# Kernel optimization log

Hardware: AMD Instinct MI355X
Metric: run time of the kernel (lower is better)

## Reference

```python
import jax, jax.numpy as jnp
import numpy as np
import math

# dims (match init_kwargs / input_specs)
T, B, S = 2048, 8, 512
D, H, DFF, NQ, W = 512, 8, 2048, 10, 16
EPS = 1e-5
NEG = -1e30


def _ln(x, g, b):
    mu = jnp.mean(x, axis=-1, keepdims=True)
    var = jnp.mean((x - mu) ** 2, axis=-1, keepdims=True)
    return (x - mu) * jax.lax.rsqrt(var + EPS) * g + b


def setup_inputs() -> dict:
    key = jax.random.key(0)
    ks = jax.random.split(key, 10)
    f = lambda k, shape, s=0.02: jax.random.normal(k, shape, jnp.float32) * s
    return {
        'tgt': jax.random.normal(ks[0], (T, B, D), jnp.float32),
        'memory': jax.random.normal(ks[1], (S, B, D), jnp.float32),
        'queries': f(ks[2], (NQ, D), 1.0 / math.sqrt(D)),
        'wk': f(ks[3], (NQ, 1), 1.0 / math.sqrt(NQ)),
        'in_proj_w': f(ks[4], (3 * D, D)),
        'in_proj_b': jnp.zeros((3 * D,), jnp.float32),
        'out_proj_w': f(ks[5], (D, D)),
        'out_proj_b': jnp.zeros((D,), jnp.float32),
        'lin1_w': f(ks[6], (DFF, D)),
        'lin1_b': jnp.zeros((DFF,), jnp.float32),
        'lin2_w': f(ks[7], (D, DFF)),
        'lin2_b': jnp.zeros((D,), jnp.float32),
        'ln1_g': jnp.ones((D,), jnp.float32), 'ln1_b': jnp.zeros((D,), jnp.float32),
        'ln2_g': jnp.ones((D,), jnp.float32), 'ln2_b': jnp.zeros((D,), jnp.float32),
        'ln3_g': jnp.ones((D,), jnp.float32), 'ln3_b': jnp.zeros((D,), jnp.float32),
    }


def _qa_block(x, queries, wk):
    # x: (T, B, D). Learned queries: per-head unit-norm + depth scale (QaN).
    dh = D // H
    q = queries.reshape(NQ, H, dh)
    q = q / (jnp.linalg.norm(q, axis=-1, keepdims=True) + 1e-6)
    q = (q / math.sqrt(dh)).reshape(NQ, D)
    # LocalAttention(window=W, look_backward=1, look_forward=1, non-causal, autopad)
    # k = v = x; T % W == 0 so autopad is a no-op.
    xb = jnp.transpose(x, (1, 0, 2))                       # (B, T, D)
    nw = T // W
    scale = D ** -0.5                                      # dim_head = D (single-head local attn)
    bk = xb.reshape(B, nw, W, D)
    pad = jnp.zeros((B, 1, W, D), x.dtype)
    bkp = jnp.concatenate([pad, bk, pad], axis=1)          # (B, nw+2, W, D)
    kv = jnp.concatenate([bkp[:, i:i + nw] for i in range(3)], axis=2)  # (B, nw, 3W, D)
    win_ok = jnp.pad(jnp.ones((nw,), bool), (1, 1))
    vm = jnp.stack([win_ok[i:i + nw] for i in range(3)], axis=1)        # (nw, 3)
    kmask = jnp.repeat(vm, W, axis=1)                                   # (nw, 3W)
    # The query vector is identical for every time step, so every position in a
    # window sees the same (query, keyset) pair -> one attention row per (n, window).
    sim = jnp.einsum('nd,bmjd->bnmj', q * scale, kv)       # (B, NQ, nw, 3W)
    sim = jnp.where(kmask[None, None], sim, NEG)
    attn = jax.nn.softmax(sim, axis=-1)
    out = jnp.einsum('bnmj,bmjd->bnmd', attn, kv)          # (B, NQ, nw, D)
    out = jnp.einsum('bnmd,n->bmd', out, wk[:, 0])         # mix N queries via wk (N,1)
    out = jnp.broadcast_to(out[:, :, None], (B, nw, W, D)).reshape(B, T, D)
    return jnp.transpose(out, (1, 0, 2))                   # (T, B, D)


def _mha_block(x, mem, in_w, in_b, out_w, out_b):
    dh = D // H
    wq, wkk, wv = jnp.split(in_w, 3, axis=0)
    bq, bk, bv = jnp.split(in_b, 3)
    q = (x @ wq.T + bq).reshape(T, B, H, dh).transpose(1, 2, 0, 3)   # (B,H,T,dh)
    k = (mem @ wkk.T + bk).reshape(S, B, H, dh).transpose(1, 2, 0, 3)
    v = (mem @ wv.T + bv).reshape(S, B, H, dh).transpose(1, 2, 0, 3)
    attn = jax.nn.softmax(jnp.einsum('bhtd,bhsd->bhts', q, k) / math.sqrt(dh), axis=-1)
    o = jnp.einsum('bhts,bhsd->bhtd', attn, v).transpose(2, 0, 1, 3).reshape(T, B, D)
    return o @ out_w.T + out_b


def reference(tgt, memory, queries, wk, in_proj_w, in_proj_b, out_proj_w, out_proj_b,
              lin1_w, lin1_b, lin2_w, lin2_b, ln1_g, ln1_b, ln2_g, ln2_b, ln3_g, ln3_b):
    # post-norm (norm_first=False), eval mode: dropouts + stochastic_depth(rate=0) are identity
    x = tgt
    x = _ln(x + _qa_block(x, queries, wk), ln1_g, ln1_b)
    x = _ln(x + _mha_block(x, memory, in_proj_w, in_proj_b, out_proj_w, out_proj_b), ln2_g, ln2_b)
    ff = jax.nn.relu(x @ lin1_w.T + lin1_b) @ lin2_w.T + lin2_b
    x = _ln(x + ff, ln3_g, ln3_b)
    # x = tgt + stochastic_depth(x - tgt) == x in eval / rate 0
    return x
```

## Files before the change

kernel.cpp:

```cpp
#include <hip/hip_runtime.h>


typedef unsigned short u16;
typedef unsigned int u32;
typedef short short8_t __attribute__((ext_vector_type(8)));
typedef float f32x4 __attribute__((ext_vector_type(4)));

#define TT 2048
#define BB 8
#define SS 512
#define DD 512
#define HH 8
#define DH 64
#define DFF 2048
#define NQ 10
#define WW 16
#define NW 128
#define KVPART 2097152

__device__ __forceinline__ float b2f(u16 u) {
    return __uint_as_float(((unsigned int)u) << 16);
}
__device__ __forceinline__ u16 f2b(float f) {
    unsigned int x = __float_as_uint(f);
    unsigned int r = x + 0x7FFFu + ((x >> 16) & 1u);
    return (u16)(r >> 16);
}
__device__ __forceinline__ u32 cvt_pk_bf16(float lo, float hi) {
    u32 r;
    asm volatile("v_cvt_pk_bf16_f32 %0, %1, %2" : "=v"(r) : "v"(lo), "v"(hi));
    return r;
}
__device__ __forceinline__ float wave_sum(float v) {
    #pragma unroll
    for (int o = 32; o > 0; o >>= 1) v += __shfl_xor(v, o, 64);
    return v;
}
__device__ __forceinline__ float wave_max(float v) {
    #pragma unroll
    for (int o = 32; o > 0; o >>= 1) v = fmaxf(v, __shfl_xor(v, o, 64));
    return v;
}
__device__ __forceinline__ void load4(const u16* p, float* v) {
    ushort4 t = *(const ushort4*)p;
    v[0] = b2f(t.x); v[1] = b2f(t.y); v[2] = b2f(t.z); v[3] = b2f(t.w);
}
__device__ __forceinline__ void load4(const float* p, float* v) {
    float4 t = *(const float4*)p;
    v[0] = t.x; v[1] = t.y; v[2] = t.z; v[3] = t.w;
}
__device__ __forceinline__ void st1(u16* p, float v) { *p = f2b(v); }
__device__ __forceinline__ void st1(float* p, float v) { *p = v; }

__device__ __forceinline__ void async16(const u16* g, u16* l) {
    __builtin_amdgcn_global_load_lds((const __attribute__((address_space(1))) u32*)g,
                                     (__attribute__((address_space(3))) u32*)l, 16, 0, 0);
}

__device__ __forceinline__ void xcd_remap(int& bx, int& by) {
    int flat = blockIdx.y * gridDim.x + blockIdx.x;
    int xcd = flat & 7;
    int j = flat >> 3;
    by = xcd * ((int)gridDim.y >> 3) + j / (int)gridDim.x;
    bx = j % (int)gridDim.x;
}

__device__ __forceinline__ void cvt_block(const float* s, u16* d, int base) {
    int i = base + threadIdx.x * 4;
    float4 v = *(const float4*)(s + i);
    ushort4 o;
    o.x = f2b(v.x); o.y = f2b(v.y); o.z = f2b(v.z); o.w = f2b(v.w);
    *(ushort4*)(d + i) = o;
}

__global__ __launch_bounds__(256) void cvt2_kernel(const float* __restrict__ s0,
                                                   const float* __restrict__ s1,
                                                   u16* __restrict__ d0,
                                                   u16* __restrict__ d1) {
    int bid = blockIdx.x;
    if (bid < 2048) cvt_block(s0, d0, bid * 1024);
    else            cvt_block(s1, d1, (bid - 2048) * 1024);
}

__global__ __launch_bounds__(256) void cvt3_kernel(const float* __restrict__ s0,
                                                   const float* __restrict__ s1,
                                                   const float* __restrict__ s2,
                                                   u16* __restrict__ d0,
                                                   u16* __restrict__ d1,
                                                   u16* __restrict__ d2) {
    int bid = blockIdx.x;
    if (bid < 256)       cvt_block(s0, d0, bid * 1024);
    else if (bid < 1280) cvt_block(s1, d1, (bid - 256) * 1024);
    else                 cvt_block(s2, d2, (bid - 1280) * 1024);
}

__global__ __launch_bounds__(512) void qeff_kernel(const float* __restrict__ queries,
                                                   float* __restrict__ qeff) {
    int d = threadIdx.x;
    const float KS = 0.0055242717280199026f;
    for (int n = 0; n < NQ; n++) {
        float v = queries[n * DD + d];
        float ss = wave_sum(v * v);
        float norm = sqrtf(ss);
        qeff[n * DD + d] = v / (norm + 1e-6f) * KS;
    }
}

__global__ __launch_bounds__(256) void p_kernel(const float* __restrict__ x,
                                                const float* __restrict__ qeff,
                                                float* __restrict__ p) {
    __shared__ float qe[NQ * DD];
    for (int i = threadIdx.x; i < NQ * DD; i += 256) qe[i] = qeff[i];
    __syncthreads();
    int b = blockIdx.x >> 9;
    int t = ((blockIdx.x & 511) << 2) + (threadIdx.x >> 6);
    int lane = threadIdx.x & 63;
    const float* xr = x + ((size_t)t * BB + b) * DD;
    float acc[NQ];
    #pragma unroll
    for (int n = 0; n < NQ; n++) acc[n] = 0.f;
    #pragma unroll
    for (int c = 0; c < 8; c++) {
        int d = c * 64 + lane;
        float xv = xr[d];
        #pragma unroll
        for (int n = 0; n < NQ; n++) acc[n] += xv * qe[n * DD + d];
    }
    #pragma unroll
    for (int n = 0; n < NQ; n++) {
        float s = wave_sum(acc[n]);
        if (lane == 0) p[((size_t)(b * NQ + n)) * TT + t] = s;
    }
}

__global__ __launch_bounds__(256) void winmix_kernel(const float* __restrict__ p,
                                                     const float* __restrict__ wk,
                                                     const float* __restrict__ x,
                                                     float* __restrict__ mixed) {
    __shared__ float As[48];
    int id = blockIdx.x;
    int b = id >> 7, m = id & 127;
    if (threadIdx.x < 64) {
        int j = threadIdx.x;
        int tj = (m - 1) * WW + j;
        bool valid = (j < 48) && (tj >= 0) && (tj < TT);
        float acc = 0.f;
        for (int n = 0; n < NQ; n++) {
            float v = valid ? p[((size_t)(b * NQ + n)) * TT + tj] : -1e30f;
            float mx = wave_max(v);
            float e = valid ? __expf(v - mx) : 0.f;
            float s = wave_sum(e);
            acc += wk[n] * (e / s);
        }
        if (j < 48) As[j] = acc;
    }
    __syncthreads();
    int d0 = threadIdx.x, d1 = threadIdx.x + 256;
    float a0 = 0.f, a1 = 0.f;
    int tb = (m - 1) * WW;
    for (int j = 0; j < 48; j++) {
        int t = tb + j;
        if ((unsigned)t < (unsigned)TT) {
            float aj = As[j];
            const float* xr = x + ((size_t)t * BB + b) * DD;
            a0 += aj * xr[d0];
            a1 += aj * xr[d1];
        }
    }
    mixed[(size_t)id * DD + d0] = a0;
    mixed[(size_t)id * DD + d1] = a1;
}

__global__ __launch_bounds__(256) void ln_qa_kernel(const float* __restrict__ a,
                                                    const float* __restrict__ mixed,
                                                    const float* __restrict__ g,
                                                    const float* __restrict__ bt,
                                                    u16* __restrict__ out) {
    int r = blockIdx.x * 4 + (threadIdx.x >> 6);
    int lane = threadIdx.x & 63;
    int t = r >> 3, b = r & 7;
    const float* ar = a + (size_t)r * DD;
    const float* mr = mixed + ((size_t)(b * NW + (t >> 4))) * DD;
    int d0 = lane * 8;
    float av[8], mv[8], gg[8], bb[8];
    load4(ar + d0, av); load4(ar + d0 + 4, av + 4);
    load4(mr + d0, mv); load4(mr + d0 + 4, mv + 4);
    load4(g + d0, gg);  load4(g + d0 + 4, gg + 4);
    load4(bt + d0, bb); load4(bt + d0 + 4, bb + 4);
    float v[8];
    float s = 0.f, s2 = 0.f;
    #pragma unroll
    for (int u = 0; u < 8; u++) { v[u] = av[u] + mv[u]; s += v[u]; s2 += v[u] * v[u]; }
    s = wave_sum(s); s2 = wave_sum(s2);
    float mu = s * (1.f / DD);
    float var = s2 * (1.f / DD) - mu * mu;
    float rs = rsqrtf(var + 1e-5f);
    #pragma unroll
    for (int u = 0; u < 8; u++) out[(size_t)r * DD + d0 + u] = f2b((v[u] - mu) * rs * gg[u] + bb[u]);
}

template <typename OT>
__global__ __launch_bounds__(256) void ln_rows_kernel(const u16* __restrict__ a,
                                                      const u16* __restrict__ bsrc,
                                                      const float* __restrict__ g,
                                                      const float* __restrict__ bt,
                                                      OT* __restrict__ out) {
    int r = blockIdx.x * 4 + (threadIdx.x >> 6);
    int lane = threadIdx.x & 63;
    const u16* ar = a + (size_t)r * DD;
    const u16* br = bsrc + (size_t)r * DD;
    int d0 = lane * 8;
    float av[8], cv[8], gg[8], bb[8];
    load4(ar + d0, av); load4(ar + d0 + 4, av + 4);
    load4(br + d0, cv); load4(br + d0 + 4, cv + 4);
    load4(g + d0, gg);  load4(g + d0 + 4, gg + 4);
    load4(bt + d0, bb); load4(bt + d0 + 4, bb + 4);
    float v[8];
    float s = 0.f, s2 = 0.f;
    #pragma unroll
    for (int u = 0; u < 8; u++) { v[u] = av[u] + cv[u]; s += v[u]; s2 += v[u] * v[u]; }
    s = wave_sum(s); s2 = wave_sum(s2);
    float mu = s * (1.f / DD);
    float var = s2 * (1.f / DD) - mu * mu;
    float rs = rsqrtf(var + 1e-5f);
    #pragma unroll
    for (int u = 0; u < 8; u++) st1(out + (size_t)r * DD + d0 + u, (v[u] - mu) * rs * gg[u] + bb[u]);
}

template <int RELU, int MT, int KV>
__global__ __launch_bounds__(256) void gemm_lds(const u16* __restrict__ A,
                                                const u16* __restrict__ W,
                                                const float* __restrict__ bias,
                                                u16* __restrict__ C,
                                                int M, int N, int K) {
    constexpr int BM = MT * 32;
    constexpr int NIA = BM / 64;
    __shared__ u16 As[2][BM * 32];
    __shared__ u16 Bs[2][128 * 32];
    int tid = threadIdx.x;
    int w = tid >> 6, lane = tid & 63;
    int n16 = lane & 15, quad = lane >> 4;
    int m0 = blockIdx.y * BM, n0 = blockIdx.x * 128;
    int wm16 = (w >> 1) * MT;
    int wn = (w & 1) * 64;

    const u16* gA[NIA];
    u16* lA[NIA];
    #pragma unroll
    for (int i = 0; i < NIA; i++) {
        int s = (w * NIA + i) * 64 + lane;
        int mb = s >> 6, kseg = (s >> 4) & 3, m = s & 15;
        gA[i] = A + (size_t)(m0 + mb * 16 + m) * K + kseg * 8;
        lA[i] = &As[0][(size_t)((w * NIA + i) * 64) * 8];
    }
    const u16* gB[2];
    u16* lB[2];
    #pragma unroll
    for (int i = 0; i < 2; i++) {
        int s = (w * 2 + i) * 64 + lane;
        int nb = s >> 6, kseg = (s >> 4) & 3, n = s & 15;
        gB[i] = W + (size_t)(n0 + nb * 16 + n) * K + kseg * 8;
        lB[i] = &Bs[0][(size_t)((w * 2 + i) * 64) * 8];
    }

    f32x4 acc[MT][4];
    #pragma unroll
    for (int i = 0; i < MT; i++)
        #pragma unroll
        for (int j = 0; j < 4; j++) acc[i][j] = (f32x4){0.f, 0.f, 0.f, 0.f};

    const int nk = K >> 5;
    #pragma unroll
    for (int i = 0; i < NIA; i++) async16(gA[i], lA[i]);
    #pragma unroll
    for (int i = 0; i < 2; i++) async16(gB[i], lB[i]);
    __syncthreads();

    for (int t = 0; t < nk; t++) {
        int cur = t & 1;
        if (t + 1 < nk) {
            int nxt = cur ^ 1;
            #pragma unroll
            for (int i = 0; i < NIA; i++) async16(gA[i] + (t + 1) * 32, lA[i] + nxt * (BM * 32));
            #pragma unroll
            for (int i = 0; i < 2; i++) async16(gB[i] + (t + 1) * 32, lB[i] + nxt * 4096);
        }
        const u16* Ac = &As[cur][0];
        const u16* Bc = &Bs[cur][0];
        short8_t af[MT], bf[4];
        #pragma unroll
        for (int im = 0; im < MT; im++)
            af[im] = *(const short8_t*)(Ac + (size_t)((wm16 + im) * 64 + lane) * 8);
        #pragma unroll
        for (int in = 0; in < 4; in++)
            bf[in] = *(const short8_t*)(Bc + (size_t)(((w & 1) * 4 + in) * 64 + lane) * 8);
        #pragma unroll
        for (int im = 0; im < MT; im++)
            #pragma unroll
            for (int in = 0; in < 4; in++)
                acc[im][in] = __builtin_amdgcn_mfma_f32_16x16x32_bf16(af[im], bf[in], acc[im][in], 0, 0, 0);
        __syncthreads();
    }

    float bia[4];
    #pragma unroll
    for (int in = 0; in < 4; in++) bia[in] = bias[n0 + wn + in * 16 + n16];
    #pragma unroll
    for (int im = 0; im < MT; im++) {
        #pragma unroll
        for (int r = 0; r < 4; r++) {
            int row = m0 + (wm16 + im) * 16 + quad * 4 + r;
            #pragma unroll
            for (int in = 0; in < 4; in++) {
                float v = acc[im][in][r] + bia[in];
                if (RELU) v = fmaxf(v, 0.f);
                if (KV) {
                    int col = n0 + wn + in * 16 + n16;
                    int part = col >> 9, h = (col >> 6) & 7, d = col & 63;
                    int s = row >> 3, bq = row & 7;
                    C[(size_t)part * KVPART + ((size_t)(bq * HH + h) * SS + s) * DH + d] = f2b(v);
                } else {
                    C[(size_t)row * N + n0 + wn + in * 16 + n16] = f2b(v);
                }
            }
        }
    }
}

__global__ __launch_bounds__(256) void attn_wp(const u16* __restrict__ qb,
                                               const u16* __restrict__ kvb,
                                               u16* __restrict__ ob) {
    __shared__ u16 Kb[2][2048];
    __shared__ u16 Vt[2][64][40];
    int tid = threadIdx.x;
    int w = tid >> 6, lane = tid & 63;
    int n16 = lane & 15, quad = lane >> 4, q8 = quad * 8;
    int xb, bh;
    xcd_remap(xb, bh);
    int b = bh >> 3, h = bh & 7;
    int q0 = xb * 128 + w * 32;

    short8_t aq[2][2];
    #pragma unroll
    for (int qt = 0; qt < 2; qt++) {
        const u16* qrow = qb + ((size_t)(q0 + qt * 16 + n16) * BB + b) * DD + h * DH;
        aq[qt][0] = *(const short8_t*)(qrow + q8);
        aq[qt][1] = *(const short8_t*)(qrow + 32 + q8);
    }

    const u16* kbase = kvb + (size_t)(b * HH + h) * (SS * DH);
    const u16* vbase = kvb + (size_t)KVPART + (size_t)(b * HH + h) * (SS * DH);

    const u16* gK = kbase + (size_t)((w >> 1) * 16 + n16) * DH + (w & 1) * 32 + q8;

    int m = lane & 15;
    int a2 = m >> 2, b2 = m & 3;
    int key0 = (b2 < 2) ? (4 * a2 + 2 * b2) : (16 + 4 * a2 + 2 * (b2 - 2));
    int kp2 = m * 2;
    int vd = w * 16 + quad * 4;
    const u16* gV = vbase + (size_t)key0 * DH + vd;

    float lsum[2] = {0.f, 0.f};
    f32x4 Oa[2][4];
    #pragma unroll
    for (int qt = 0; qt < 2; qt++)
        #pragma unroll
        for (int ot = 0; ot < 4; ot++) Oa[qt][ot] = (f32x4){0.f, 0.f, 0.f, 0.f};

    union VU { ushort4 q; u16 h[4]; };
    union PU { u32 wd[4]; short8_t s8; };

    {
        async16(gK, &Kb[0][w * 512]);
        VU va, vb2;
        va.q  = *(const ushort4*)(gV);
        vb2.q = *(const ushort4*)(gV + DH);
        #pragma unroll
        for (int u = 0; u < 4; u++)
            *(u32*)&Vt[0][vd + u][kp2] = (u32)va.h[u] | ((u32)vb2.h[u] << 16);
    }
    __syncthreads();

    for (int c = 0; c < 16; c++) {
        int cur = c & 1, nxt = cur ^ 1;

        VU va, vb2;
        if (c < 15) {
            const u16* gVc = gV + (size_t)(c + 1) * 32 * DH;
            va.q  = *(const ushort4*)(gVc);
            vb2.q = *(const ushort4*)(gVc + DH);
            async16(gK + (size_t)(c + 1) * 32 * DH, &Kb[nxt][w * 512]);
        }

        short8_t bk0 = *(const short8_t*)&Kb[cur][0 * 512 + lane * 8];
        short8_t bk1 = *(const short8_t*)&Kb[cur][1 * 512 + lane * 8];
        short8_t bk2 = *(const short8_t*)&Kb[cur][2 * 512 + lane * 8];
        short8_t bk3 = *(const short8_t*)&Kb[cur][3 * 512 + lane * 8];

        #pragma unroll
        for (int qt = 0; qt < 2; qt++) {
            f32x4 s0 = (f32x4){0.f, 0.f, 0.f, 0.f};
            s0 = __builtin_amdgcn_mfma_f32_16x16x32_bf16(bk0, aq[qt][0], s0, 0, 0, 0);
            s0 = __builtin_amdgcn_mfma_f32_16x16x32_bf16(bk1, aq[qt][1], s0, 0, 0, 0);
            f32x4 s1 = (f32x4){0.f, 0.f, 0.f, 0.f};
            s1 = __builtin_amdgcn_mfma_f32_16x16x32_bf16(bk2, aq[qt][0], s1, 0, 0, 0);
            s1 = __builtin_amdgcn_mfma_f32_16x16x32_bf16(bk3, aq[qt][1], s1, 0, 0, 0);

            float p0 = __expf(s0[0] * 0.125f - 8.0f);
            float p1 = __expf(s0[1] * 0.125f - 8.0f);
            float p2 = __expf(s0[2] * 0.125f - 8.0f);
            float p3 = __expf(s0[3] * 0.125f - 8.0f);
            float p4 = __expf(s1[0] * 0.125f - 8.0f);
            float p5 = __expf(s1[1] * 0.125f - 8.0f);
            float p6 = __expf(s1[2] * 0.125f - 8.0f);
            float p7 = __expf(s1[3] * 0.125f - 8.0f);
            lsum[qt] += ((p0 + p1) + (p2 + p3)) + ((p4 + p5) + (p6 + p7));

            PU pu;
            pu.wd[0] = cvt_pk_bf16(p0, p1);
            pu.wd[1] = cvt_pk_bf16(p2, p3);
            pu.wd[2] = cvt_pk_bf16(p4, p5);
            pu.wd[3] = cvt_pk_bf16(p6, p7);

            #pragma unroll
            for (int ot = 0; ot < 4; ot++) {
                short8_t bv = *(const short8_t*)&Vt[cur][ot * 16 + n16][q8];
                Oa[qt][ot] = __builtin_amdgcn_mfma_f32_16x16x32_bf16(pu.s8, bv, Oa[qt][ot], 0, 0, 0);
            }
        }

        if (c < 15) {
            #pragma unroll
            for (int u = 0; u < 4; u++)
                *(u32*)&Vt[nxt][vd + u][kp2] = (u32)va.h[u] | ((u32)vb2.h[u] << 16);
        }
        __syncthreads();
    }

    #pragma unroll
    for (int qt = 0; qt < 2; qt++) {
        float l = lsum[qt];
        l += __shfl_xor(l, 16, 64);
        l += __shfl_xor(l, 32, 64);
        #pragma unroll
        for (int r = 0; r < 4; r++) {
            float lq = __shfl(l, quad * 4 + r, 64);
            float inv = 1.f / lq;
            int t = q0 + qt * 16 + quad * 4 + r;
            u16* orow = ob + ((size_t)t * BB + b) * DD + h * DH + n16;
            #pragma unroll
            for (int ot = 0; ot < 4; ot++) orow[ot * 16] = f2b(Oa[qt][ot][r] * inv);
        }
    }
}

extern "C" void kernel_launch(void* const* d_in, const int* in_sizes, int n_in,
                              void* d_out, int out_size, void* d_ws, size_t ws_size,
                              hipStream_t stream) {
    const float* tgt       = (const float*)d_in[0];
    const float* memory    = (const float*)d_in[1];
    const float* queries   = (const float*)d_in[2];
    const float* wk        = (const float*)d_in[3];
    const float* in_proj_w = (const float*)d_in[4];
    const float* in_proj_b = (const float*)d_in[5];
    const float* out_proj_w= (const float*)d_in[6];
    const float* out_proj_b= (const float*)d_in[7];
    const float* lin1_w    = (const float*)d_in[8];
    const float* lin1_b    = (const float*)d_in[9];
    const float* lin2_w    = (const float*)d_in[10];
    const float* lin2_b    = (const float*)d_in[11];
    const float* ln1_g     = (const float*)d_in[12];
    const float* ln1_b     = (const float*)d_in[13];
    const float* ln2_g     = (const float*)d_in[14];
    const float* ln2_b     = (const float*)d_in[15];
    const float* ln3_g     = (const float*)d_in[16];
    const float* ln3_b     = (const float*)d_in[17];

    char* w = (char*)d_ws;
    float* qeff  = (float*)(w + 0);
    float* pbuf  = (float*)(w + 20480);
    float* mixed = (float*)(w + 872448);
    u16* y1  = (u16*)(w + 2969600);
    u16* qb  = (u16*)(w + 19746816);
    u16* kvb = (u16*)(w + 36524032);
    u16* ob  = (u16*)(w + 44912640);
    u16* ipwb = (u16*)(w + 44912640);
    u16* memb = (u16*)(w + 46485504);
    u16* opwb = (u16*)(w + 36524032);
    u16* l1wb = (u16*)(w + 37048320);
    u16* l2wb = (u16*)(w + 39145472);
    u16* t1 = qb;
    u16* y2 = ob;
    u16* hb = qb;
    u16* fb = y1;

    cvt2_kernel<<<2816, 256, 0, stream>>>(memory, in_proj_w, memb, ipwb);

    qeff_kernel<<<1, 512, 0, stream>>>(queries, qeff);
    p_kernel<<<BB * (TT / 4), 256, 0, stream>>>(tgt, qeff, pbuf);
    winmix_kernel<<<BB * NW, 256, 0, stream>>>(pbuf, wk, tgt, mixed);
    ln_qa_kernel<<<(TT * BB) / 4, 256, 0, stream>>>(tgt, mixed, ln1_g, ln1_b, y1);

    gemm_lds<0, 4, 0><<<dim3(DD / 128, (TT * BB) / 128), 256, 0, stream>>>(y1, ipwb, in_proj_b, qb, TT * BB, DD, DD);
    gemm_lds<0, 4, 1><<<dim3(1024 / 128, (SS * BB) / 128), 256, 0, stream>>>(memb, ipwb + (size_t)DD * DD, in_proj_b + DD, kvb, SS * BB, 1024, DD);
    attn_wp<<<dim3(TT / 128, BB * HH), 256, 0, stream>>>(qb, kvb, ob);
    cvt3_kernel<<<2304, 256, 0, stream>>>(out_proj_w, lin1_w, lin2_w, opwb, l1wb, l2wb);
    gemm_lds<0, 4, 0><<<dim3(DD / 128, (TT * BB) / 128), 256, 0, stream>>>(ob, opwb, out_proj_b, t1, TT * BB, DD, DD);
    ln_rows_kernel<u16><<<(TT * BB) / 4, 256, 0, stream>>>(y1, t1, ln2_g, ln2_b, y2);

    for (int c = 0; c < 4; c++) {
        const u16* y2c = y2 + (size_t)c * 4096 * DD;
        u16* fbc = fb + (size_t)c * 4096 * DD;
        gemm_lds<1, 4, 0><<<dim3(DFF / 128, 4096 / 128), 256, 0, stream>>>(y2c, l1wb, lin1_b, hb, 4096, DFF, DD);
        gemm_lds<0, 2, 0><<<dim3(DD / 128, 4096 / 64), 256, 0, stream>>>(hb, l2wb, lin2_b, fbc, 4096, DD, DFF);
    }
    ln_rows_kernel<float><<<(TT * BB) / 4, 256, 0, stream>>>(y2, fb, ln3_g, ln3_b, (float*)d_out);
}
```

Measured before the change: 538.6 us.

## Add 64x64-tile triple-buffered GEMM for KV projection and FFN down-projection

Adds a new GEMM kernel with 64x64 output tiles, each wave computing a 2x2 grid of 16x16 MFMA tiles. It uses a three-stage async LDS buffer with explicit vmcnt waits, so loads for step t+2 run while step t computes. The KV projection and the lin2 GEMM switch to it, which launches more blocks for these small-N or long-K shapes. The cost is less data reuse per tile and more global traffic for A and W.

```diff
diff --git a/kernel.cpp b/kernel.cpp
--- a/kernel.cpp
+++ b/kernel.cpp
@@ -312,6 +312,93 @@
             int row = m0 + (wm16 + im) * 16 + quad * 4 + r;
             #pragma unroll
             for (int in = 0; in < 4; in++) {
+                float v = acc[im][in][r] + bia[in];
+                if (RELU) v = fmaxf(v, 0.f);
+                if (KV) {
+                    int col = n0 + wn + in * 16 + n16;
+                    int part = col >> 9, h = (col >> 6) & 7, d = col & 63;
+                    int s = row >> 3, bq = row & 7;
+                    C[(size_t)part * KVPART + ((size_t)(bq * HH + h) * SS + s) * DH + d] = f2b(v);
+                } else {
+                    C[(size_t)row * N + n0 + wn + in * 16 + n16] = f2b(v);
+                }
+            }
+        }
+    }
+}
+
+template <int RELU, int KV>
+__global__ __launch_bounds__(256) void gemm_np(const u16* __restrict__ A,
+                                               const u16* __restrict__ W,
+                                               const float* __restrict__ bias,
+                                               u16* __restrict__ C,
+                                               int M, int N, int K) {
+    __shared__ u16 As[3][64 * 32];
+    __shared__ u16 Bs[3][64 * 32];
+    int tid = threadIdx.x;
+    int w = tid >> 6, lane = tid & 63;
+    int n16 = lane & 15, quad = lane >> 4;
+    int m0 = blockIdx.y * 64, n0 = blockIdx.x * 64;
+    int wm16 = (w >> 1) * 2;
+    int wn = (w & 1) * 32;
+
+    const u16* gA0 = A + (size_t)(m0 + w * 16 + n16) * K + quad * 8;
+    const u16* gB0 = W + (size_t)(n0 + w * 16 + n16) * K + quad * 8;
+
+    f32x4 acc[2][2];
+    #pragma unroll
+    for (int i = 0; i < 2; i++)
+        #pragma unroll
+        for (int j = 0; j < 2; j++) acc[i][j] = (f32x4){0.f, 0.f, 0.f, 0.f};
+
+    const int nk = K >> 5;
+    async16(gA0, &As[0][w * 512]);
+    async16(gB0, &Bs[0][w * 512]);
+    async16(gA0 + 32, &As[1][w * 512]);
+    async16(gB0 + 32, &Bs[1][w * 512]);
+
+    int cur = 0;
+    for (int t = 0; t < nk; t++) {
+        if (t + 1 < nk) {
+            __asm__ volatile("s_waitcnt vmcnt(2)" ::: "memory");
+        } else {
+            __asm__ volatile("s_waitcnt vmcnt(0)" ::: "memory");
+        }
+        __builtin_amdgcn_s_barrier();
+        __builtin_amdgcn_sched_barrier(0);
+        if (t + 2 < nk) {
+            int nx2 = cur + 2; if (nx2 >= 3) nx2 -= 3;
+            async16(gA0 + (t + 2) * 32, &As[nx2][w * 512]);
+            async16(gB0 + (t + 2) * 32, &Bs[nx2][w * 512]);
+        }
+        const u16* Ac = &As[cur][0];
+        const u16* Bc = &Bs[cur][0];
+        short8_t af[2], bf[2];
+        #pragma unroll
+        for (int im = 0; im < 2; im++)
+            af[im] = *(const short8_t*)(Ac + (size_t)((wm16 + im) * 64 + lane) * 8);
+        #pragma unroll
+        for (int in = 0; in < 2; in++)
+            bf[in] = *(const short8_t*)(Bc + (size_t)(((w & 1) * 2 + in) * 64 + lane) * 8);
+        #pragma unroll
+        for (int im = 0; im < 2; im++)
+            #pragma unroll
+            for (int in = 0; in < 2; in++)
+                acc[im][in] = __builtin_amdgcn_mfma_f32_16x16x32_bf16(af[im], bf[in], acc[im][in], 0, 0, 0);
+        __asm__ volatile("s_waitcnt lgkmcnt(0)" ::: "memory");
+        cur = (cur == 2) ? 0 : cur + 1;
+    }
+
+    float bia[2];
+    #pragma unroll
+    for (int in = 0; in < 2; in++) bia[in] = bias[n0 + wn + in * 16 + n16];
+    #pragma unroll
+    for (int im = 0; im < 2; im++) {
+        #pragma unroll
+        for (int r = 0; r < 4; r++) {
+            int row = m0 + (wm16 + im) * 16 + quad * 4 + r;
+            #pragma unroll
+            for (int in = 0; in < 2; in++) {
                 float v = acc[im][in][r] + bia[in];
                 if (RELU) v = fmaxf(v, 0.f);
                 if (KV) {
@@ -502,7 +589,7 @@
     ln_qa_kernel<<<(TT * BB) / 4, 256, 0, stream>>>(tgt, mixed, ln1_g, ln1_b, y1);
 
     gemm_lds<0, 4, 0><<<dim3(DD / 128, (TT * BB) / 128), 256, 0, stream>>>(y1, ipwb, in_proj_b, qb, TT * BB, DD, DD);
-    gemm_lds<0, 4, 1><<<dim3(1024 / 128, (SS * BB) / 128), 256, 0, stream>>>(memb, ipwb + (size_t)DD * DD, in_proj_b + DD, kvb, SS * BB, 1024, DD);
+    gemm_np<0, 1><<<dim3(1024 / 64, (SS * BB) / 64), 256, 0, stream>>>(memb, ipwb + (size_t)DD * DD, in_proj_b + DD, kvb, SS * BB, 1024, DD);
     attn_wp<<<dim3(TT / 128, BB * HH), 256, 0, stream>>>(qb, kvb, ob);
     cvt3_kernel<<<2304, 256, 0, stream>>>(out_proj_w, lin1_w, lin2_w, opwb, l1wb, l2wb);
     gemm_lds<0, 4, 0><<<dim3(DD / 128, (TT * BB) / 128), 256, 0, stream>>>(ob, opwb, out_proj_b, t1, TT * BB, DD, DD);
@@ -512,7 +599,7 @@
         const u16* y2c = y2 + (size_t)c * 4096 * DD;
         u16* fbc = fb + (size_t)c * 4096 * DD;
         gemm_lds<1, 4, 0><<<dim3(DFF / 128, 4096 / 128), 256, 0, stream>>>(y2c, l1wb, lin1_b, hb, 4096, DFF, DD);
-        gemm_lds<0, 2, 0><<<dim3(DD / 128, 4096 / 64), 256, 0, stream>>>(hb, l2wb, lin2_b, fbc, 4096, DD, DFF);
+        gemm_np<0, 0><<<dim3(DD / 64, 4096 / 64), 256, 0, stream>>>(hb, l2wb, lin2_b, fbc, 4096, DD, DFF);
     }
     ln_rows_kernel<float><<<(TT * BB) / 4, 256, 0, stream>>>(y2, fb, ln3_g, ln3_b, (float*)d_out);
 }
```

Measured after the change: 533.5 us. About the same (-0.9%).
